# Kernel tuning notes

Measured on AMD Instinct MI355X. Metric: run time of the kernel, lower is better.

The kernel has to match this reference:

```python
import jax, jax.numpy as jnp
import numpy as np

B = 32          # decode batch (one query token per sequence)
HID = 4096      # hidden_size
H = 32          # num_heads
D = 128         # head_dim
BLK = 16        # KV-cache block size (vLLM default)
MAXB = 64       # max blocks per sequence
NBLK = 2048     # total cache blocks
S = MAXB * BLK  # max context length = 1024
ROPE_THETA = 10000.0


def _rope(x, positions):
    # x: [B, H, D], positions: [B] int. GPT-NeoX / Llama half-split rotary.
    half = D // 2
    inv_freq = 1.0 / (ROPE_THETA ** (jnp.arange(0, half, dtype=jnp.float32) / half))
    freqs = positions.astype(jnp.float32)[:, None] * inv_freq[None, :]  # [B, D/2]
    cos = jnp.cos(freqs)[:, None, :]  # [B, 1, D/2]
    sin = jnp.sin(freqs)[:, None, :]
    x1, x2 = x[..., :half], x[..., half:]
    return jnp.concatenate([x1 * cos - x2 * sin, x1 * sin + x2 * cos], axis=-1)


def setup_inputs() -> dict:
    key = jax.random.key(0)
    ks = jax.random.split(key, 8)
    hidden_states = jax.random.normal(ks[0], (B, HID), jnp.float32)
    Wq = jax.random.normal(ks[1], (HID, HID), jnp.float32) * 0.02
    Wk = jax.random.normal(ks[2], (HID, HID), jnp.float32) * 0.02
    Wv = jax.random.normal(ks[3], (HID, HID), jnp.float32) * 0.02
    Wo = jax.random.normal(ks[4], (HID, HID), jnp.float32) * 0.02
    k_cache = jax.random.normal(ks[5], (NBLK, BLK, H, D), jnp.float32)
    v_cache = jax.random.normal(ks[6], (NBLK, BLK, H, D), jnp.float32)
    # each sequence owns MAXB distinct cache blocks (non-contiguous)
    block_tables = jax.random.permutation(ks[7], NBLK)[: B * MAXB].reshape(B, MAXB).astype(jnp.int32)
    context_lens = jax.random.randint(jax.random.fold_in(key, 9), (B,), S // 2, S + 1).astype(jnp.int32)
    positions = context_lens - 1  # current token position
    slot_mapping = (block_tables[jnp.arange(B), positions // BLK] * BLK + positions % BLK).astype(jnp.int32)
    return dict(hidden_states=hidden_states, k_cache=k_cache, v_cache=v_cache,
                Wq=Wq, Wk=Wk, Wv=Wv, Wo=Wo,
                positions=positions, slot_mapping=slot_mapping,
                block_tables=block_tables, context_lens=context_lens)


def reference(hidden_states, k_cache, v_cache, Wq, Wk, Wv, Wo,
              positions, slot_mapping, block_tables, context_lens):
    # QKV projections (bias-free, torch Linear convention: x @ W.T)
    q = (hidden_states @ Wq.T).reshape(B, H, D)
    k = (hidden_states @ Wk.T).reshape(B, H, D)
    v = (hidden_states @ Wv.T).reshape(B, H, D)
    q = _rope(q, positions)
    k = _rope(k, positions)
    # write new k/v into the paged cache at slot_mapping
    kc = k_cache.reshape(NBLK * BLK, H, D).at[slot_mapping].set(k)
    vc = v_cache.reshape(NBLK * BLK, H, D).at[slot_mapping].set(v)
    kc = kc.reshape(NBLK, BLK, H, D)
    vc = vc.reshape(NBLK, BLK, H, D)
    # paged gather: [B, MAXB, BLK, H, D] -> [B, S, H, D]
    keys = kc[block_tables].reshape(B, S, H, D)
    vals = vc[block_tables].reshape(B, S, H, D)
    scores = jnp.einsum('bhd,bshd->bhs', q, keys) * (D ** -0.5)
    valid = jnp.arange(S)[None, :] < context_lens[:, None]  # [B, S]
    scores = jnp.where(valid[:, None, :], scores, jnp.float32(-1e30))
    probs = jax.nn.softmax(scores, axis=-1)
    attn = jnp.einsum('bhs,bshd->bhd', probs, vals).reshape(B, H * D)
    return attn @ Wo.T
```

## Files before the change

### kernel.cpp

```cpp
#include <hip/hip_runtime.h>
#include <math.h>

#define HID 4096
#define B 32
#define H 32
#define D 128
#define KBLK 16
#define MAXB 64
#define S_MAX 1024

__global__ __launch_bounds__(256) void gemv_kernel(
    const float* __restrict__ W0, const float* __restrict__ W1, const float* __restrict__ W2,
    const float* __restrict__ x, float* __restrict__ out)
{
    __shared__ float wt[8][256];
    const int bid = blockIdx.x;
    const int mat = bid >> 9;
    const int n0 = (bid & 511) << 3;
    const float* W = (mat == 0) ? W0 : ((mat == 1) ? W1 : W2);
    float* outp = out + (size_t)mat * (B * HID);

    const int tid = threadIdx.x;
    const int lane = tid & 63;
    const int wid = tid >> 6;
    const int b0 = wid << 3;

    float acc[8][8];
#pragma unroll
    for (int c = 0; c < 8; ++c)
#pragma unroll
        for (int j = 0; j < 8; ++j) acc[c][j] = 0.f;

    for (int k0 = 0; k0 < HID; k0 += 256) {
        __syncthreads();
#pragma unroll
        for (int i = 0; i < 2; ++i) {
            int idx = tid + i * 256;
            int row = idx >> 6;
            int c4 = idx & 63;
            float4 v = *reinterpret_cast<const float4*>(
                &W[(size_t)(n0 + row) * HID + k0 + (c4 << 2)]);
            *reinterpret_cast<float4*>(&wt[row][c4 << 2]) = v;
        }
        __syncthreads();

        float4 hs4[8];
#pragma unroll
        for (int j = 0; j < 8; ++j)
            hs4[j] = *reinterpret_cast<const float4*>(
                &x[(size_t)(b0 + j) * HID + k0 + (lane << 2)]);

#pragma unroll
        for (int c = 0; c < 8; ++c) {
            float4 w4 = *reinterpret_cast<const float4*>(&wt[c][lane << 2]);
#pragma unroll
            for (int j = 0; j < 8; ++j) {
                acc[c][j] += w4.x * hs4[j].x;
                acc[c][j] += w4.y * hs4[j].y;
                acc[c][j] += w4.z * hs4[j].z;
                acc[c][j] += w4.w * hs4[j].w;
            }
        }
    }

#pragma unroll
    for (int m = 1; m < 64; m <<= 1) {
#pragma unroll
        for (int c = 0; c < 8; ++c)
#pragma unroll
            for (int j = 0; j < 8; ++j)
                acc[c][j] += __shfl_xor(acc[c][j], m, 64);
    }
    float myval = 0.f;
#pragma unroll
    for (int c = 0; c < 8; ++c)
#pragma unroll
        for (int j = 0; j < 8; ++j)
            myval = (lane == (c * 8 + j)) ? acc[c][j] : myval;
    const int oc = lane >> 3;
    const int oj = lane & 7;
    outp[(size_t)(b0 + oj) * HID + n0 + oc] = myval;
}

__global__ __launch_bounds__(64) void rope_kernel(float* __restrict__ qkv,
                                                  const int* __restrict__ positions)
{
    const int bh = blockIdx.x;
    const int b = bh >> 5;
    const int h = bh & 31;
    const int d = threadIdx.x;
    const float pos = (float)positions[b];
    const float inv = exp2f(-(float)d * 0.20762050593046013f);
    const float f = pos * inv;
    const float cs = cosf(f);
    const float sn = sinf(f);
#pragma unroll
    for (int mat = 0; mat < 2; ++mat) {
        float* base = qkv + (size_t)mat * (B * HID) + (size_t)b * HID + h * D;
        float x1 = base[d];
        float x2 = base[d + 64];
        base[d] = x1 * cs - x2 * sn;
        base[d + 64] = x1 * sn + x2 * cs;
    }
}

__global__ __launch_bounds__(256) void attn_kernel(
    const float* __restrict__ qkv,
    const float* __restrict__ k_cache,
    const float* __restrict__ v_cache,
    const int* __restrict__ block_tables,
    const int* __restrict__ context_lens,
    const int* __restrict__ positions,
    float* __restrict__ attn_out)
{
    const int h = blockIdx.x;
    const int b = blockIdx.y;
    const int tid = threadIdx.x;
    const int L = context_lens[b];
    const int pos = positions[b];

    __shared__ float sc[S_MAX];
    __shared__ float red[8];
    __shared__ int btl[MAXB];
    __shared__ float o4[4][D];

    if (tid < MAXB) btl[tid] = block_tables[b * MAXB + tid];
    __syncthreads();

    const float* qptr = qkv + (size_t)b * HID + h * D;
    const float* knew = qkv + (size_t)(B * HID) + (size_t)b * HID + h * D;
    const float* vnew = qkv + (size_t)(2 * B * HID) + (size_t)b * HID + h * D;
    const float scale = 0.088388347648318447f;

    const int hw = tid >> 5;
    const int hl = tid & 31;
    const float4 qv = *reinterpret_cast<const float4*>(qptr + (hl << 2));

    int s = hw;
    for (; s + 8 < L; s += 16) {
        const int s1 = s + 8;
        const float* kp0 = (s == pos) ? knew
            : k_cache + ((size_t)(btl[s >> 4] * KBLK + (s & 15)) * H + h) * D;
        const float* kp1 = (s1 == pos) ? knew
            : k_cache + ((size_t)(btl[s1 >> 4] * KBLK + (s1 & 15)) * H + h) * D;
        float4 k0 = *reinterpret_cast<const float4*>(kp0 + (hl << 2));
        float4 k1 = *reinterpret_cast<const float4*>(kp1 + (hl << 2));
        float d0 = qv.x * k0.x + qv.y * k0.y + qv.z * k0.z + qv.w * k0.w;
        float d1 = qv.x * k1.x + qv.y * k1.y + qv.z * k1.z + qv.w * k1.w;
#pragma unroll
        for (int m = 16; m; m >>= 1) {
            d0 += __shfl_xor(d0, m, 64);
            d1 += __shfl_xor(d1, m, 64);
        }
        if (hl == 0) { sc[s] = d0 * scale; sc[s1] = d1 * scale; }
    }
    for (; s < L; s += 8) {
        const float* kp = (s == pos) ? knew
            : k_cache + ((size_t)(btl[s >> 4] * KBLK + (s & 15)) * H + h) * D;
        float4 k0 = *reinterpret_cast<const float4*>(kp + (hl << 2));
        float d0 = qv.x * k0.x + qv.y * k0.y + qv.z * k0.z + qv.w * k0.w;
#pragma unroll
        for (int m = 16; m; m >>= 1) d0 += __shfl_xor(d0, m, 64);
        if (hl == 0) sc[s] = d0 * scale;
    }
    __syncthreads();

    float lmax = -1e30f;
    for (int i = tid; i < L; i += 256) lmax = fmaxf(lmax, sc[i]);
#pragma unroll
    for (int m = 32; m; m >>= 1) lmax = fmaxf(lmax, __shfl_xor(lmax, m, 64));
    if ((tid & 63) == 0) red[tid >> 6] = lmax;
    __syncthreads();
    const float gmax = fmaxf(fmaxf(red[0], red[1]), fmaxf(red[2], red[3]));

    float lsum = 0.f;
    for (int i = tid; i < L; i += 256) {
        float p = __expf(sc[i] - gmax);
        sc[i] = p;
        lsum += p;
    }
#pragma unroll
    for (int m = 32; m; m >>= 1) lsum += __shfl_xor(lsum, m, 64);
    if ((tid & 63) == 0) red[4 + (tid >> 6)] = lsum;
    __syncthreads();
    const float inv = 1.f / (red[4] + red[5] + red[6] + red[7]);

    const int w = tid >> 6;
    const int l2 = (tid & 63) << 1;
    float accx = 0.f, accy = 0.f;
    s = w;
    for (; s + 4 < L; s += 8) {
        const int s1 = s + 4;
        const float* vp0 = (s == pos) ? vnew
            : v_cache + ((size_t)(btl[s >> 4] * KBLK + (s & 15)) * H + h) * D;
        const float* vp1 = (s1 == pos) ? vnew
            : v_cache + ((size_t)(btl[s1 >> 4] * KBLK + (s1 & 15)) * H + h) * D;
        float2 v0 = *reinterpret_cast<const float2*>(vp0 + l2);
        float2 v1 = *reinterpret_cast<const float2*>(vp1 + l2);
        float p0 = sc[s], p1 = sc[s1];
        accx += p0 * v0.x; accy += p0 * v0.y;
        accx += p1 * v1.x; accy += p1 * v1.y;
    }
    for (; s < L; s += 4) {
        const float* vp = (s == pos) ? vnew
            : v_cache + ((size_t)(btl[s >> 4] * KBLK + (s & 15)) * H + h) * D;
        float2 v0 = *reinterpret_cast<const float2*>(vp + l2);
        float p0 = sc[s];
        accx += p0 * v0.x; accy += p0 * v0.y;
    }
    o4[w][l2] = accx;
    o4[w][l2 + 1] = accy;
    __syncthreads();
    if (tid < D) {
        float o = (o4[0][tid] + o4[1][tid] + o4[2][tid] + o4[3][tid]) * inv;
        attn_out[(size_t)b * HID + h * D + tid] = o;
    }
}

extern "C" void kernel_launch(void* const* d_in, const int* in_sizes, int n_in,
                              void* d_out, int out_size, void* d_ws, size_t ws_size,
                              hipStream_t stream) {
    const float* hs        = (const float*)d_in[0];
    const float* k_cache   = (const float*)d_in[1];
    const float* v_cache   = (const float*)d_in[2];
    const float* Wq        = (const float*)d_in[3];
    const float* Wk        = (const float*)d_in[4];
    const float* Wv        = (const float*)d_in[5];
    const float* Wo        = (const float*)d_in[6];
    const int*   positions = (const int*)d_in[7];
    const int*   block_tables = (const int*)d_in[9];
    const int*   context_lens = (const int*)d_in[10];
    float* out = (float*)d_out;

    float* qkv = (float*)d_ws;
    float* attn_ws = qkv + (size_t)3 * B * HID;

    gemv_kernel<<<dim3(3 * 512), 256, 0, stream>>>(Wq, Wk, Wv, hs, qkv);
    rope_kernel<<<dim3(B * H), 64, 0, stream>>>(qkv, positions);
    attn_kernel<<<dim3(H, B), 256, 0, stream>>>(qkv, k_cache, v_cache,
                                                block_tables, context_lens, positions, attn_ws);
    gemv_kernel<<<dim3(512), 256, 0, stream>>>(Wo, Wo, Wo, attn_ws, out);
}
```

Before: 288.3 us.

## Split attention across context chunks with a split-K combine kernel

Splits each (batch, head) attention into up to four 256-token chunks, launched as separate blocks that each produce a partial max, sum and output vector. A new combine kernel merges the partials with log-sum-exp rescaling. The aim is to raise parallelism from 1024 blocks to up to 4096 so more CUs stay busy while streaming the KV cache. The cost is an extra kernel launch and a small workspace round trip.

```diff
diff --git a/kernel.cpp b/kernel.cpp
--- a/kernel.cpp
+++ b/kernel.cpp
@@ -8,6 +8,8 @@
 #define KBLK 16
 #define MAXB 64
 #define S_MAX 1024
+#define CHUNK 256
+#define NCHUNK 4
 
 __global__ __launch_bounds__(256) void gemv_kernel(
     const float* __restrict__ W0, const float* __restrict__ W1, const float* __restrict__ W2,
@@ -104,27 +106,33 @@
     }
 }
 
-__global__ __launch_bounds__(256) void attn_kernel(
+__global__ __launch_bounds__(256) void attn_partial_kernel(
     const float* __restrict__ qkv,
     const float* __restrict__ k_cache,
     const float* __restrict__ v_cache,
     const int* __restrict__ block_tables,
     const int* __restrict__ context_lens,
     const int* __restrict__ positions,
-    float* __restrict__ attn_out)
+    float* __restrict__ pm,
+    float* __restrict__ pl,
+    float* __restrict__ po)
 {
     const int h = blockIdx.x;
-    const int b = blockIdx.y;
+    const int c = blockIdx.y;
+    const int b = blockIdx.z;
+    const int L = context_lens[b];
+    const int s0 = c << 8;
+    if (s0 >= L) return;
+    const int Lc = min(L - s0, CHUNK);
+    const int pos = positions[b];
     const int tid = threadIdx.x;
-    const int L = context_lens[b];
-    const int pos = positions[b];
-
-    __shared__ float sc[S_MAX];
+
+    __shared__ float sc[CHUNK];
     __shared__ float red[8];
-    __shared__ int btl[MAXB];
+    __shared__ int btl[16];
     __shared__ float o4[4][D];
 
-    if (tid < MAXB) btl[tid] = block_tables[b * MAXB + tid];
+    if (tid < 16) btl[tid] = block_tables[b * MAXB + (c << 4) + tid];
     __syncthreads();
 
     const float* qptr = qkv + (size_t)b * HID + h * D;
@@ -136,13 +144,13 @@
     const int hl = tid & 31;
     const float4 qv = *reinterpret_cast<const float4*>(qptr + (hl << 2));
 
-    int s = hw;
-    for (; s + 8 < L; s += 16) {
-        const int s1 = s + 8;
-        const float* kp0 = (s == pos) ? knew
-            : k_cache + ((size_t)(btl[s >> 4] * KBLK + (s & 15)) * H + h) * D;
-        const float* kp1 = (s1 == pos) ? knew
-            : k_cache + ((size_t)(btl[s1 >> 4] * KBLK + (s1 & 15)) * H + h) * D;
+    int i = hw;
+    for (; i + 8 < Lc; i += 16) {
+        const int sA = s0 + i, sB = s0 + i + 8;
+        const float* kp0 = (sA == pos) ? knew
+            : k_cache + ((size_t)(btl[i >> 4] * KBLK + (sA & 15)) * H + h) * D;
+        const float* kp1 = (sB == pos) ? knew
+            : k_cache + ((size_t)(btl[(i + 8) >> 4] * KBLK + (sB & 15)) * H + h) * D;
         float4 k0 = *reinterpret_cast<const float4*>(kp0 + (hl << 2));
         float4 k1 = *reinterpret_cast<const float4*>(kp1 + (hl << 2));
         float d0 = qv.x * k0.x + qv.y * k0.y + qv.z * k0.z + qv.w * k0.w;
@@ -152,69 +160,95 @@
             d0 += __shfl_xor(d0, m, 64);
             d1 += __shfl_xor(d1, m, 64);
         }
-        if (hl == 0) { sc[s] = d0 * scale; sc[s1] = d1 * scale; }
-    }
-    for (; s < L; s += 8) {
-        const float* kp = (s == pos) ? knew
-            : k_cache + ((size_t)(btl[s >> 4] * KBLK + (s & 15)) * H + h) * D;
+        if (hl == 0) { sc[i] = d0 * scale; sc[i + 8] = d1 * scale; }
+    }
+    for (; i < Lc; i += 8) {
+        const int sA = s0 + i;
+        const float* kp = (sA == pos) ? knew
+            : k_cache + ((size_t)(btl[i >> 4] * KBLK + (sA & 15)) * H + h) * D;
         float4 k0 = *reinterpret_cast<const float4*>(kp + (hl << 2));
         float d0 = qv.x * k0.x + qv.y * k0.y + qv.z * k0.z + qv.w * k0.w;
 #pragma unroll
         for (int m = 16; m; m >>= 1) d0 += __shfl_xor(d0, m, 64);
-        if (hl == 0) sc[s] = d0 * scale;
-    }
-    __syncthreads();
-
-    float lmax = -1e30f;
-    for (int i = tid; i < L; i += 256) lmax = fmaxf(lmax, sc[i]);
-#pragma unroll
-    for (int m = 32; m; m >>= 1) lmax = fmaxf(lmax, __shfl_xor(lmax, m, 64));
-    if ((tid & 63) == 0) red[tid >> 6] = lmax;
-    __syncthreads();
-    const float gmax = fmaxf(fmaxf(red[0], red[1]), fmaxf(red[2], red[3]));
-
-    float lsum = 0.f;
-    for (int i = tid; i < L; i += 256) {
-        float p = __expf(sc[i] - gmax);
-        sc[i] = p;
-        lsum += p;
-    }
-#pragma unroll
-    for (int m = 32; m; m >>= 1) lsum += __shfl_xor(lsum, m, 64);
-    if ((tid & 63) == 0) red[4 + (tid >> 6)] = lsum;
-    __syncthreads();
-    const float inv = 1.f / (red[4] + red[5] + red[6] + red[7]);
+        if (hl == 0) sc[i] = d0 * scale;
+    }
+    for (; i < CHUNK; i += 8)
+        if (hl == 0) sc[i] = -1e30f;
+    __syncthreads();
 
     const int w = tid >> 6;
+    const float x = sc[tid];
+    float m = x;
+#pragma unroll
+    for (int mm = 32; mm; mm >>= 1) m = fmaxf(m, __shfl_xor(m, mm, 64));
+    if ((tid & 63) == 0) red[w] = m;
+    __syncthreads();
+    const float gm = fmaxf(fmaxf(red[0], red[1]), fmaxf(red[2], red[3]));
+
+    float p = (x > -1e29f) ? __expf(x - gm) : 0.f;
+    sc[tid] = p;
+    float l = p;
+#pragma unroll
+    for (int mm = 32; mm; mm >>= 1) l += __shfl_xor(l, mm, 64);
+    if ((tid & 63) == 0) red[4 + w] = l;
+    __syncthreads();
+    const float gl = red[4] + red[5] + red[6] + red[7];
+
     const int l2 = (tid & 63) << 1;
     float accx = 0.f, accy = 0.f;
-    s = w;
-    for (; s + 4 < L; s += 8) {
-        const int s1 = s + 4;
-        const float* vp0 = (s == pos) ? vnew
-            : v_cache + ((size_t)(btl[s >> 4] * KBLK + (s & 15)) * H + h) * D;
-        const float* vp1 = (s1 == pos) ? vnew
-            : v_cache + ((size_t)(btl[s1 >> 4] * KBLK + (s1 & 15)) * H + h) * D;
+    i = w;
+    for (; i + 4 < Lc; i += 8) {
+        const int sA = s0 + i, sB = s0 + i + 4;
+        const float* vp0 = (sA == pos) ? vnew
+            : v_cache + ((size_t)(btl[i >> 4] * KBLK + (sA & 15)) * H + h) * D;
+        const float* vp1 = (sB == pos) ? vnew
+            : v_cache + ((size_t)(btl[(i + 4) >> 4] * KBLK + (sB & 15)) * H + h) * D;
         float2 v0 = *reinterpret_cast<const float2*>(vp0 + l2);
         float2 v1 = *reinterpret_cast<const float2*>(vp1 + l2);
-        float p0 = sc[s], p1 = sc[s1];
+        float p0 = sc[i], p1 = sc[i + 4];
         accx += p0 * v0.x; accy += p0 * v0.y;
         accx += p1 * v1.x; accy += p1 * v1.y;
     }
-    for (; s < L; s += 4) {
-        const float* vp = (s == pos) ? vnew
-            : v_cache + ((size_t)(btl[s >> 4] * KBLK + (s & 15)) * H + h) * D;
+    for (; i < Lc; i += 4) {
+        const float* vp = (s0 + i == pos) ? vnew
+            : v_cache + ((size_t)(btl[i >> 4] * KBLK + ((s0 + i) & 15)) * H + h) * D;
         float2 v0 = *reinterpret_cast<const float2*>(vp + l2);
-        float p0 = sc[s];
+        float p0 = sc[i];
         accx += p0 * v0.x; accy += p0 * v0.y;
     }
     o4[w][l2] = accx;
     o4[w][l2 + 1] = accy;
     __syncthreads();
+
+    const int bh = b * H + h;
     if (tid < D) {
-        float o = (o4[0][tid] + o4[1][tid] + o4[2][tid] + o4[3][tid]) * inv;
-        attn_out[(size_t)b * HID + h * D + tid] = o;
-    }
+        float o = o4[0][tid] + o4[1][tid] + o4[2][tid] + o4[3][tid];
+        po[((size_t)bh * NCHUNK + c) * D + tid] = o;
+    } else if (tid == D) {
+        pm[bh * NCHUNK + c] = gm;
+        pl[bh * NCHUNK + c] = gl;
+    }
+}
+
+__global__ __launch_bounds__(128) void attn_combine_kernel(
+    const float* __restrict__ pm, const float* __restrict__ pl,
+    const float* __restrict__ po, const int* __restrict__ context_lens,
+    float* __restrict__ attn_out)
+{
+    const int bh = blockIdx.x;
+    const int b = bh >> 5;
+    const int tid = threadIdx.x;
+    const int nc = (context_lens[b] + CHUNK - 1) >> 8;
+
+    float m = -1e30f;
+    for (int c = 0; c < nc; ++c) m = fmaxf(m, pm[bh * NCHUNK + c]);
+    float wsum = 0.f, o = 0.f;
+    for (int c = 0; c < nc; ++c) {
+        float wc = __expf(pm[bh * NCHUNK + c] - m);
+        wsum += wc * pl[bh * NCHUNK + c];
+        o += wc * po[((size_t)bh * NCHUNK + c) * D + tid];
+    }
+    attn_out[(size_t)bh * D + tid] = o / wsum;
 }
 
 extern "C" void kernel_launch(void* const* d_in, const int* in_sizes, int n_in,
@@ -232,12 +266,16 @@
     const int*   context_lens = (const int*)d_in[10];
     float* out = (float*)d_out;
 
-    float* qkv = (float*)d_ws;
+    float* qkv     = (float*)d_ws;
     float* attn_ws = qkv + (size_t)3 * B * HID;
+    float* pm      = attn_ws + (size_t)B * HID;
+    float* pl      = pm + (size_t)B * H * NCHUNK;
+    float* po      = pl + (size_t)B * H * NCHUNK;
 
     gemv_kernel<<<dim3(3 * 512), 256, 0, stream>>>(Wq, Wk, Wv, hs, qkv);
     rope_kernel<<<dim3(B * H), 64, 0, stream>>>(qkv, positions);
-    attn_kernel<<<dim3(H, B), 256, 0, stream>>>(qkv, k_cache, v_cache,
-                                                block_tables, context_lens, positions, attn_ws);
+    attn_partial_kernel<<<dim3(H, NCHUNK, B), 256, 0, stream>>>(
+        qkv, k_cache, v_cache, block_tables, context_lens, positions, pm, pl, po);
+    attn_combine_kernel<<<dim3(B * H), 128, 0, stream>>>(pm, pl, po, context_lens, attn_ws);
     gemv_kernel<<<dim3(512), 256, 0, stream>>>(Wo, Wo, Wo, attn_ws, out);
 }
```

New measurement: 267.3 us. -7.3%, faster.
